# Performance work log

Measured on AMD Instinct MI355X. Metric: run time of the kernel, lower is better.

## Reference

```python
import jax, jax.numpy as jnp
import numpy as np

N = 50000
E = 800000
IN_DIM, HID, LAT, DEC_HID = 256, 256, 128, 512


def _glorot(key, shape):
    fan_in, fan_out = shape
    lim = np.sqrt(6.0 / (fan_in + fan_out))
    return jax.random.uniform(key, shape, jnp.float32, -lim, lim)


def setup_inputs() -> dict:
    key = jax.random.key(0)
    ks = jax.random.split(key, 10)
    x = jax.random.normal(ks[0], (N, IN_DIM), jnp.float32)
    edge_index = jax.random.randint(ks[1], (2, E), 0, N, dtype=jnp.int64)
    return {
        "x": x,
        "edge_index": edge_index,
        "W1": _glorot(ks[2], (IN_DIM, HID)), "b1": jnp.zeros((HID,), jnp.float32),
        "W2": _glorot(ks[3], (HID, LAT)), "b2": jnp.zeros((LAT,), jnp.float32),
        "Wd1": _glorot(ks[4], (LAT, DEC_HID)), "bd1": jnp.zeros((DEC_HID,), jnp.float32),
        "Wd2": _glorot(ks[5], (DEC_HID, IN_DIM)), "bd2": jnp.zeros((IN_DIM,), jnp.float32),
    }


def _gcn_layer(x, src, dst, W, b, num_nodes):
    # linear transform
    xt = x @ W + b                      # [N, out]
    # scatter-mean aggregation over incoming edges (PyG aggr='mean')
    msg = xt[src]                       # [E, out] gather of source features
    summed = jax.ops.segment_sum(msg, dst, num_segments=num_nodes)
    cnt = jax.ops.segment_sum(jnp.ones((src.shape[0],), xt.dtype), dst,
                              num_segments=num_nodes)
    mean = summed / jnp.maximum(cnt, 1.0)[:, None]   # 0 for isolated nodes
    # relu + residual
    return jax.nn.relu(mean) + xt


def reference(x, edge_index, W1, b1, W2, b2, Wd1, bd1, Wd2, bd2):
    src, dst = edge_index[0], edge_index[1]
    h = _gcn_layer(x, src, dst, W1, b1, x.shape[0])
    z = _gcn_layer(h, src, dst, W2, b2, x.shape[0])
    # decoder MLP
    x_hat = jax.nn.relu(z @ Wd1 + bd1) @ Wd2 + bd2
    return (x_hat, z)
```

## Files before the change

kernel.cpp:

```cpp
#include <hip/hip_runtime.h>
#include <hip/hip_bf16.h>

#define TPB 256

typedef __attribute__((ext_vector_type(8))) short short8;
typedef __attribute__((ext_vector_type(4))) float f32x4;

__device__ __forceinline__ unsigned short f2bf(float f) {
    unsigned int u = __float_as_uint(f);
    u = (u + 0x7FFFu + ((u >> 16) & 1u)) >> 16;
    return (unsigned short)u;
}
__device__ __forceinline__ float bflo(unsigned int u) { return __uint_as_float(u << 16); }
__device__ __forceinline__ float bfhi(unsigned int u) { return __uint_as_float(u & 0xFFFF0000u); }

__device__ __forceinline__ void gload16(const void* g, void* l) {
    __builtin_amdgcn_global_load_lds(
        (const __attribute__((address_space(1))) unsigned int*)g,
        (__attribute__((address_space(3))) unsigned int*)l, 16, 0, 0);
}

__global__ void transpose_convert_all(
    const float* __restrict__ Wa, unsigned short* __restrict__ Ta, int Ka, int Na,
    const float* __restrict__ Wb, unsigned short* __restrict__ Tb, int Kb, int Nb,
    const float* __restrict__ Wc, unsigned short* __restrict__ Tc, int Kc, int Nc_,
    const float* __restrict__ Wd, unsigned short* __restrict__ Td, int Kd, int Nd)
{
    __shared__ float tile[32][33];
    int b = blockIdx.x;
    const float* W; unsigned short* T; int K, Nn;
    const int ta = (Na / 32) * (Ka / 32);
    const int tb = (Nb / 32) * (Kb / 32);
    const int tc = (Nc_ / 32) * (Kc / 32);
    if (b < ta)                { W = Wa; T = Ta; K = Ka; Nn = Na; }
    else if (b < ta + tb)      { b -= ta;           W = Wb; T = Tb; K = Kb; Nn = Nb; }
    else if (b < ta + tb + tc) { b -= ta + tb;      W = Wc; T = Tc; K = Kc; Nn = Nc_; }
    else                       { b -= ta + tb + tc; W = Wd; T = Td; K = Kd; Nn = Nd; }
    const int nx = Nn / 32;
    const int n0 = (b % nx) * 32;
    const int k0 = (b / nx) * 32;
    const int tx = threadIdx.x, ty = threadIdx.y;
#pragma unroll
    for (int i = 0; i < 4; ++i)
        tile[ty + i * 8][tx] = W[(size_t)(k0 + ty + i * 8) * Nn + n0 + tx];
    __syncthreads();
#pragma unroll
    for (int i = 0; i < 4; ++i)
        T[(size_t)(n0 + ty + i * 8) * K + k0 + tx] = f2bf(tile[tx][ty + i * 8]);
}

__device__ __forceinline__ void load_a16f(const float* p, short8& lo, short8& hi) {
    float4 f0 = *reinterpret_cast<const float4*>(p);
    float4 f1 = *reinterpret_cast<const float4*>(p + 4);
    float4 f2 = *reinterpret_cast<const float4*>(p + 8);
    float4 f3 = *reinterpret_cast<const float4*>(p + 12);
    lo[0] = (short)f2bf(f0.x); lo[1] = (short)f2bf(f0.y);
    lo[2] = (short)f2bf(f0.z); lo[3] = (short)f2bf(f0.w);
    lo[4] = (short)f2bf(f1.x); lo[5] = (short)f2bf(f1.y);
    lo[6] = (short)f2bf(f1.z); lo[7] = (short)f2bf(f1.w);
    hi[0] = (short)f2bf(f2.x); hi[1] = (short)f2bf(f2.y);
    hi[2] = (short)f2bf(f2.z); hi[3] = (short)f2bf(f2.w);
    hi[4] = (short)f2bf(f3.x); hi[5] = (short)f2bf(f3.y);
    hi[6] = (short)f2bf(f3.z); hi[7] = (short)f2bf(f3.w);
}

__device__ __forceinline__ void copy_out32(unsigned short* C, const float* Cst, const float* bias,
                                           int rowbase, int bn, int M, int Nc, int t, bool doRelu) {
#pragma unroll
    for (int it = 0; it < 2; ++it) {
        const int idx = it * 2048 + t * 8;
        const int row = idx >> 7, col = idx & 127;
        const int m = rowbase + row;
        if (m >= M) continue;
        float4 v0 = *reinterpret_cast<const float4*>(&Cst[idx]);
        float4 v1 = *reinterpret_cast<const float4*>(&Cst[idx + 4]);
        float4 b0 = *reinterpret_cast<const float4*>(&bias[bn + col]);
        float4 b1 = *reinterpret_cast<const float4*>(&bias[bn + col + 4]);
        float o[8] = {v0.x + b0.x, v0.y + b0.y, v0.z + b0.z, v0.w + b0.w,
                      v1.x + b1.x, v1.y + b1.y, v1.z + b1.z, v1.w + b1.w};
        short8 s;
#pragma unroll
        for (int j = 0; j < 8; ++j) {
            const float vv = doRelu ? fmaxf(o[j], 0.f) : o[j];
            s[j] = (short)f2bf(vv);
        }
        *reinterpret_cast<short8*>(&C[(size_t)m * Nc + bn + col]) = s;
    }
}
__device__ __forceinline__ void copy_out32(float* C, const float* Cst, const float* bias,
                                           int rowbase, int bn, int M, int Nc, int t, bool doRelu) {
#pragma unroll
    for (int it = 0; it < 4; ++it) {
        const int idx = it * 1024 + t * 4;
        const int row = idx >> 7, col = idx & 127;
        const int m = rowbase + row;
        if (m >= M) continue;
        float4 v = *reinterpret_cast<const float4*>(&Cst[idx]);
        float4 b = *reinterpret_cast<const float4*>(&bias[bn + col]);
        v.x += b.x; v.y += b.y; v.z += b.z; v.w += b.w;
        if (doRelu) {
            v.x = fmaxf(v.x, 0.f); v.y = fmaxf(v.y, 0.f);
            v.z = fmaxf(v.z, 0.f); v.w = fmaxf(v.w, 0.f);
        }
        *reinterpret_cast<float4*>(&C[(size_t)m * Nc + bn + col]) = v;
    }
}

template <typename TA, typename TC, int K, bool RELU>
__global__ __launch_bounds__(256) void mfma_gemm4(
    const TA* __restrict__ A, const unsigned short* __restrict__ Bt,
    const float* __restrict__ bias, TC* __restrict__ C, int M, int Nc)
{
    __shared__ unsigned short lds_s[2][12288];
    constexpr bool AF32 = (sizeof(TA) == 4);

    const int t  = threadIdx.x;
    const int l  = t & 63;
    const int w  = t >> 6;
    const int wm = w >> 1, wn = w & 1;
    const int bm = blockIdx.x * 64;
    const int bn = blockIdx.y * 128;

    f32x4 acc[2][4] = {};

    const int r4 = t >> 2;
    const int q4 = t & 3;
    const int gmr = bm + r4;
    short8 sa0, sa1;

    auto loadAregs = [&](int k0) {
        if (gmr < M) load_a16f((const float*)A + (size_t)gmr * K + k0 + q4 * 16, sa0, sa1);
        else { sa0 = (short8)0; sa1 = (short8)0; }
    };
    auto writeAregs = [&](int buf) {
        const int s0 = (2 * q4)     ^ (r4 & 7);
        const int s1 = (2 * q4 + 1) ^ (r4 & 7);
        *reinterpret_cast<short8*>(&lds_s[buf][r4 * 64 + s0 * 8]) = sa0;
        *reinterpret_cast<short8*>(&lds_s[buf][r4 * 64 + s1 * 8]) = sa1;
    };
    auto stageA_lds = [&](int buf, int k0) {
#pragma unroll
        for (int ii = 0; ii < 2; ++ii) {
            const int seg = w + ii * 4;
            const int rr  = seg * 8 + (l >> 3);
            const int ss  = l & 7;
            const int gr  = min(bm + rr, M - 1);
            gload16((const unsigned short*)A + (size_t)gr * K + k0 + ((ss ^ (rr & 7)) * 8),
                    &lds_s[buf][seg * 512]);
        }
    };
    auto stageB = [&](int buf, int k0) {
#pragma unroll
        for (int ii = 0; ii < 4; ++ii) {
            const int seg = w + ii * 4;
            const int rr  = seg * 8 + (l >> 3);
            const int ss  = l & 7;
            gload16(Bt + (size_t)(bn + rr) * K + k0 + ((ss ^ (rr & 7)) * 8),
                    &lds_s[buf][4096 + seg * 512]);
        }
    };

    constexpr int S = K / 64;

    if (AF32) {
        loadAregs(0);
        writeAregs(0);
        if (S > 1) loadAregs(64);
    } else {
        stageA_lds(0, 0);
    }
    stageB(0, 0);
    __syncthreads();

#pragma unroll
    for (int step = 0; step < S; ++step) {
        const int k0  = step * 64;
        const int cur = step & 1;

        if (step + 1 < S) {
            if (AF32) writeAregs(cur ^ 1);
            else      stageA_lds(cur ^ 1, k0 + 64);
            stageB(cur ^ 1, k0 + 64);
        }
        if (AF32 && step + 2 < S) loadAregs(k0 + 128);

#pragma unroll
        for (int kk = 0; kk < 2; ++kk) {
            short8 af[2], bf4[4];
#pragma unroll
            for (int mf = 0; mf < 2; ++mf) {
                const int row  = wm * 32 + mf * 16 + (l & 15);
                const int slot = (kk * 4 + (l >> 4)) ^ (row & 7);
                af[mf] = *reinterpret_cast<const short8*>(&lds_s[cur][row * 64 + slot * 8]);
            }
#pragma unroll
            for (int nf = 0; nf < 4; ++nf) {
                const int row  = wn * 64 + nf * 16 + (l & 15);
                const int slot = (kk * 4 + (l >> 4)) ^ (row & 7);
                bf4[nf] = *reinterpret_cast<const short8*>(&lds_s[cur][4096 + row * 64 + slot * 8]);
            }
#pragma unroll
            for (int mf = 0; mf < 2; ++mf)
#pragma unroll
                for (int nf = 0; nf < 4; ++nf)
                    acc[mf][nf] = __builtin_amdgcn_mfma_f32_16x16x32_bf16(
                        af[mf], bf4[nf], acc[mf][nf], 0, 0, 0);
        }
        __syncthreads();
    }

    float* Cst = reinterpret_cast<float*>(lds_s);
#pragma unroll
    for (int p = 0; p < 2; ++p) {
        if (wm == p) {
#pragma unroll
            for (int mf = 0; mf < 2; ++mf)
#pragma unroll
                for (int nf = 0; nf < 4; ++nf)
#pragma unroll
                    for (int rr = 0; rr < 4; ++rr) {
                        const int row = mf * 16 + (l >> 4) * 4 + rr;
                        const int col = wn * 64 + nf * 16 + (l & 15);
                        Cst[row * 128 + col] = acc[mf][nf][rr];
                    }
        }
        __syncthreads();
        copy_out32(C, Cst, bias, bm + p * 32, bn, M, Nc, t, RELU);
        if (p == 0) __syncthreads();
    }
}

__global__ void hist_kernel(const int* __restrict__ dst, int* __restrict__ counts, int E)
{
    int e = blockIdx.x * TPB + threadIdx.x;
    if (e < E) atomicAdd(&counts[dst[e]], 1);
}

__global__ void scan1_kernel(const int* __restrict__ counts,
                             int* __restrict__ local, int* __restrict__ bsum, int N)
{
    __shared__ int sh[TPB];
    const int t = threadIdx.x;
    const int base = blockIdx.x * 1024 + t * 4;
    int v[4];
#pragma unroll
    for (int i = 0; i < 4; ++i) v[i] = (base + i < N) ? counts[base + i] : 0;
    const int s = v[0] + v[1] + v[2] + v[3];
    sh[t] = s;
    __syncthreads();
    for (int d = 1; d < TPB; d <<= 1) {
        int x = (t >= d) ? sh[t - d] : 0;
        __syncthreads();
        sh[t] += x;
        __syncthreads();
    }
    int run = sh[t] - s;
#pragma unroll
    for (int i = 0; i < 4; ++i) {
        if (base + i < N) local[base + i] = run;
        run += v[i];
    }
    if (t == TPB - 1) bsum[blockIdx.x] = sh[TPB - 1];
}

__global__ void scan2_kernel(int* __restrict__ bsum, int nb)
{
    __shared__ int sh[TPB];
    const int t = threadIdx.x;
    const int v = (t < nb) ? bsum[t] : 0;
    sh[t] = v;
    __syncthreads();
    for (int d = 1; d < TPB; d <<= 1) {
        int x = (t >= d) ? sh[t - d] : 0;
        __syncthreads();
        sh[t] += x;
        __syncthreads();
    }
    if (t < nb) bsum[t] = sh[t] - v;
}

__global__ void scan3_kernel(int* __restrict__ offsets, int* __restrict__ cursor,
                             const int* __restrict__ bsum, int N)
{
    const int i = blockIdx.x * TPB + threadIdx.x;
    if (i < N) {
        const int o = offsets[i] + bsum[i >> 10];
        offsets[i] = o;
        cursor[i]  = o;
    }
}

__global__ void build_perm_kernel(const int* __restrict__ src, const int* __restrict__ dst,
                                  int* __restrict__ cursor, int* __restrict__ perm, int E)
{
    int e = blockIdx.x * TPB + threadIdx.x;
    if (e < E) {
        int pos = atomicAdd(&cursor[dst[e]], 1);
        perm[pos] = src[e];
    }
}

template <int F, int CH, bool WRITE_ZF32>
__global__ __launch_bounds__(256) void agg_kernel(
    const uint2* __restrict__ xt,
    const int* __restrict__ offsets, const int* __restrict__ counts,
    const int* __restrict__ perm,
    uint2* __restrict__ out, float* __restrict__ zf32, int N)
{
    constexpr int RU  = F / 4;
    constexpr int L   = RU / CH;
    constexpr int NPB = TPB / L;

    const int chunk = blockIdx.x % CH;
    const int node  = (blockIdx.x / CH) * NPB + threadIdx.x / L;
    const int g     = threadIdx.x % L;
    if (node >= N) return;
    const int col = chunk * L + g;

    const int start = offsets[node];
    const int deg   = counts[node];

    float a0 = 0.f, a1 = 0.f, a2 = 0.f, a3 = 0.f;

    for (int base = 0; base < deg; base += L) {
        const int m = min(L, deg - base);
        const int pidx = perm[start + base + ((g < m) ? g : (m - 1))];
        int j = 0;
        for (; j + 4 <= m; j += 4) {
            const int s0 = __shfl(pidx, j + 0, L);
            const int s1 = __shfl(pidx, j + 1, L);
            const int s2 = __shfl(pidx, j + 2, L);
            const int s3 = __shfl(pidx, j + 3, L);
            const uint2 v0 = xt[(size_t)s0 * RU + col];
            const uint2 v1 = xt[(size_t)s1 * RU + col];
            const uint2 v2 = xt[(size_t)s2 * RU + col];
            const uint2 v3 = xt[(size_t)s3 * RU + col];
            a0 += bflo(v0.x) + bflo(v1.x) + bflo(v2.x) + bflo(v3.x);
            a1 += bfhi(v0.x) + bfhi(v1.x) + bfhi(v2.x) + bfhi(v3.x);
            a2 += bflo(v0.y) + bflo(v1.y) + bflo(v2.y) + bflo(v3.y);
            a3 += bfhi(v0.y) + bfhi(v1.y) + bfhi(v2.y) + bfhi(v3.y);
        }
        for (; j < m; ++j) {
            const int s = __shfl(pidx, j, L);
            const uint2 v = xt[(size_t)s * RU + col];
            a0 += bflo(v.x); a1 += bfhi(v.x);
            a2 += bflo(v.y); a3 += bfhi(v.y);
        }
    }

    const float c = (float)max(deg, 1);
    const uint2 xv = xt[(size_t)node * RU + col];
    const float r0 = fmaxf(a0 / c, 0.f) + bflo(xv.x);
    const float r1 = fmaxf(a1 / c, 0.f) + bfhi(xv.x);
    const float r2 = fmaxf(a2 / c, 0.f) + bflo(xv.y);
    const float r3 = fmaxf(a3 / c, 0.f) + bfhi(xv.y);

    uint2 o;
    o.x = (unsigned int)f2bf(r0) | ((unsigned int)f2bf(r1) << 16);
    o.y = (unsigned int)f2bf(r2) | ((unsigned int)f2bf(r3) << 16);
    out[(size_t)node * RU + col] = o;
    if (WRITE_ZF32) {
        float4 z4 = make_float4(r0, r1, r2, r3);
        *reinterpret_cast<float4*>(&zf32[(size_t)node * F + 4 * col]) = z4;
    }
}

extern "C" void kernel_launch(void* const* d_in, const int* in_sizes, int n_in,
                              void* d_out, int out_size, void* d_ws, size_t ws_size,
                              hipStream_t stream)
{
    const int IN_DIM = 256, HID = 256, LAT = 128, DEC_HID = 512;
    const int N = in_sizes[0] / IN_DIM;
    const int E = in_sizes[1] / 2;

    const float* x   = (const float*)d_in[0];
    const int*   ei  = (const int*)d_in[1];
    const float* W1  = (const float*)d_in[2];
    const float* b1  = (const float*)d_in[3];
    const float* W2  = (const float*)d_in[4];
    const float* b2  = (const float*)d_in[5];
    const float* Wd1 = (const float*)d_in[6];
    const float* bd1 = (const float*)d_in[7];
    const float* Wd2 = (const float*)d_in[8];
    const float* bd2 = (const float*)d_in[9];

    const int* src = ei;
    const int* dst = ei + E;

    unsigned short* xt1  = (unsigned short*)d_ws;
    unsigned short* h    = xt1  + (size_t)N * 256;
    unsigned short* xt2  = h    + (size_t)N * 256;
    unsigned short* zbf  = xt2  + (size_t)N * 128;
    unsigned short* hdec = zbf  + (size_t)N * 128;
    unsigned short* wt1  = hdec + (size_t)N * 512;
    unsigned short* wt2  = wt1  + 256 * 256;
    unsigned short* wtd1 = wt2  + 128 * 256;
    unsigned short* wtd2 = wtd1 + 512 * 128;
    int* counts  = (int*)(wtd2 + 256 * 512);
    int* offsets = counts + N;
    int* cursor  = offsets + N;
    int* bsum    = cursor + N;
    int* perm    = bsum + 256;

    float* out_xhat = (float*)d_out;
    float* out_z    = out_xhat + (size_t)N * IN_DIM;

    dim3 blk(TPB);
    const int egrid = (E + TPB - 1) / TPB;
    const int mb64 = (N + 63) / 64;
    const int nscan = (N + 1023) / 1024;

    {
        const int tiles = (HID/32)*(IN_DIM/32) + (LAT/32)*(HID/32)
                        + (DEC_HID/32)*(LAT/32) + (IN_DIM/32)*(DEC_HID/32);
        transpose_convert_all<<<tiles, dim3(32, 8), 0, stream>>>(
            W1, wt1, IN_DIM, HID,  W2, wt2, HID, LAT,
            Wd1, wtd1, LAT, DEC_HID,  Wd2, wtd2, DEC_HID, IN_DIM);
    }

    hipMemsetAsync(counts, 0, (size_t)N * 4, stream);
    hist_kernel<<<egrid, blk, 0, stream>>>(dst, counts, E);
    scan1_kernel<<<nscan, blk, 0, stream>>>(counts, offsets, bsum, N);
    scan2_kernel<<<1, blk, 0, stream>>>(bsum, nscan);
    scan3_kernel<<<(N + TPB - 1) / TPB, blk, 0, stream>>>(offsets, cursor, bsum, N);
    build_perm_kernel<<<egrid, blk, 0, stream>>>(src, dst, cursor, perm, E);

    mfma_gemm4<float, unsigned short, 256, false><<<dim3(mb64, HID / 128), blk, 0, stream>>>(
        x, wt1, b1, xt1, N, HID);
    {
        const int ngroups = (N + 15) / 16;
        agg_kernel<256, 4, false><<<ngroups * 4, blk, 0, stream>>>(
            (const uint2*)xt1, offsets, counts, perm, (uint2*)h, nullptr, N);
    }

    mfma_gemm4<unsigned short, unsigned short, 256, false><<<dim3(mb64, LAT / 128), blk, 0, stream>>>(
        h, wt2, b2, xt2, N, LAT);
    {
        const int ngroups = (N + 7) / 8;
        agg_kernel<128, 1, true><<<ngroups, blk, 0, stream>>>(
            (const uint2*)xt2, offsets, counts, perm, (uint2*)zbf, out_z, N);
    }

    mfma_gemm4<unsigned short, unsigned short, 128, true><<<dim3(mb64, DEC_HID / 128), blk, 0, stream>>>(
        zbf, wtd1, bd1, hdec, N, DEC_HID);
    mfma_gemm4<unsigned short, float, 512, false><<<dim3(mb64, IN_DIM / 128), blk, 0, stream>>>(
        hdec, wtd2, bd2, out_xhat, N, IN_DIM);
}
```

Measured before the change: 277.7 us.

## Partition histogram and permutation builds by destination chunk; widen layer-1 aggregation split

The histogram and CSR permutation kernels now launch eight blocks per edge tile. Each block reads dst four at a time with int4 loads and only does atomics for destinations in its own eighth of the node range, which is meant to localize atomic traffic per XCD or cache slice. The cost is that every edge index is read eight times. Separately, the first aggregation kernel now splits each node's features into 8 chunks instead of 4, raising parallelism per node.

```diff
diff --git a/kernel.cpp b/kernel.cpp
--- a/kernel.cpp
+++ b/kernel.cpp
@@ -230,10 +230,25 @@
     }
 }
 
-__global__ void hist_kernel(const int* __restrict__ dst, int* __restrict__ counts, int E)
-{
-    int e = blockIdx.x * TPB + threadIdx.x;
-    if (e < E) atomicAdd(&counts[dst[e]], 1);
+__global__ void hist_kernel(const int* __restrict__ dst, int* __restrict__ counts,
+                            int E, int csz)
+{
+    const int chunk = blockIdx.x & 7;
+    const int blk   = blockIdx.x >> 3;
+    const int lo = chunk * csz, hi = lo + csz;
+    const int base = (blk * TPB + threadIdx.x) * 4;
+    if (base + 3 < E) {
+        int4 d4 = *reinterpret_cast<const int4*>(dst + base);
+        if (d4.x >= lo && d4.x < hi) atomicAdd(&counts[d4.x], 1);
+        if (d4.y >= lo && d4.y < hi) atomicAdd(&counts[d4.y], 1);
+        if (d4.z >= lo && d4.z < hi) atomicAdd(&counts[d4.z], 1);
+        if (d4.w >= lo && d4.w < hi) atomicAdd(&counts[d4.w], 1);
+    } else {
+        for (int e = base; e < E; ++e) {
+            const int d = dst[e];
+            if (d >= lo && d < hi) atomicAdd(&counts[d], 1);
+        }
+    }
 }
 
 __global__ void scan1_kernel(const int* __restrict__ counts,
@@ -291,12 +306,24 @@
 }
 
 __global__ void build_perm_kernel(const int* __restrict__ src, const int* __restrict__ dst,
-                                  int* __restrict__ cursor, int* __restrict__ perm, int E)
-{
-    int e = blockIdx.x * TPB + threadIdx.x;
-    if (e < E) {
-        int pos = atomicAdd(&cursor[dst[e]], 1);
-        perm[pos] = src[e];
+                                  int* __restrict__ cursor, int* __restrict__ perm,
+                                  int E, int csz)
+{
+    const int chunk = blockIdx.x & 7;
+    const int blk   = blockIdx.x >> 3;
+    const int lo = chunk * csz, hi = lo + csz;
+    const int base = (blk * TPB + threadIdx.x) * 4;
+    if (base + 3 < E) {
+        int4 d4 = *reinterpret_cast<const int4*>(dst + base);
+        if (d4.x >= lo && d4.x < hi) { int p = atomicAdd(&cursor[d4.x], 1); perm[p] = src[base + 0]; }
+        if (d4.y >= lo && d4.y < hi) { int p = atomicAdd(&cursor[d4.y], 1); perm[p] = src[base + 1]; }
+        if (d4.z >= lo && d4.z < hi) { int p = atomicAdd(&cursor[d4.z], 1); perm[p] = src[base + 2]; }
+        if (d4.w >= lo && d4.w < hi) { int p = atomicAdd(&cursor[d4.w], 1); perm[p] = src[base + 3]; }
+    } else {
+        for (int e = base; e < E; ++e) {
+            const int d = dst[e];
+            if (d >= lo && d < hi) { int p = atomicAdd(&cursor[d], 1); perm[p] = src[e]; }
+        }
     }
 }
 
@@ -406,9 +433,10 @@
     float* out_z    = out_xhat + (size_t)N * IN_DIM;
 
     dim3 blk(TPB);
-    const int egrid = (E + TPB - 1) / TPB;
     const int mb64 = (N + 63) / 64;
     const int nscan = (N + 1023) / 1024;
+    const int csz = (N + 7) / 8;
+    const int egrid8 = ((E + TPB * 4 - 1) / (TPB * 4)) * 8;
 
     {
         const int tiles = (HID/32)*(IN_DIM/32) + (LAT/32)*(HID/32)
@@ -419,17 +447,17 @@
     }
 
     hipMemsetAsync(counts, 0, (size_t)N * 4, stream);
-    hist_kernel<<<egrid, blk, 0, stream>>>(dst, counts, E);
+    hist_kernel<<<egrid8, blk, 0, stream>>>(dst, counts, E, csz);
     scan1_kernel<<<nscan, blk, 0, stream>>>(counts, offsets, bsum, N);
     scan2_kernel<<<1, blk, 0, stream>>>(bsum, nscan);
     scan3_kernel<<<(N + TPB - 1) / TPB, blk, 0, stream>>>(offsets, cursor, bsum, N);
-    build_perm_kernel<<<egrid, blk, 0, stream>>>(src, dst, cursor, perm, E);
+    build_perm_kernel<<<egrid8, blk, 0, stream>>>(src, dst, cursor, perm, E, csz);
 
     mfma_gemm4<float, unsigned short, 256, false><<<dim3(mb64, HID / 128), blk, 0, stream>>>(
         x, wt1, b1, xt1, N, HID);
     {
-        const int ngroups = (N + 15) / 16;
-        agg_kernel<256, 4, false><<<ngroups * 4, blk, 0, stream>>>(
+        const int ngroups = (N + 31) / 32;
+        agg_kernel<256, 8, false><<<ngroups * 8, blk, 0, stream>>>(
             (const uint2*)xt1, offsets, counts, perm, (uint2*)h, nullptr, N);
     }
 
```

Measured after the change: 293.3 us. +5.6%, slower.
